# Kernel optimization log

Measured on AMD Instinct MI355X. Metric: run time of the kernel, lower is better.

## Reference

```python
import jax, jax.numpy as jnp
import numpy as np

EMBED = 768
HEADS = 12
HEAD_DIM = EMBED // HEADS

def setup_inputs() -> dict:
    key = jax.random.key(0)
    k1, k2, k3, k4 = jax.random.split(key, 4)
    x = jax.random.normal(k1, (8, 1024, EMBED), dtype=jnp.float32)
    # qkv Linear (no bias per qkv_bias=False); proj Linear with bias
    w_qkv = jax.random.normal(k2, (EMBED, 3 * EMBED), dtype=jnp.float32) * 0.02
    w_proj = jax.random.normal(k3, (EMBED, EMBED), dtype=jnp.float32) * 0.02
    b_proj = jax.random.normal(k4, (EMBED,), dtype=jnp.float32) * 0.02
    return {"x": x, "w_qkv": w_qkv, "w_proj": w_proj, "b_proj": b_proj}

def reference(x, w_qkv, w_proj, b_proj):
    b, n, e = x.shape
    h, d = HEADS, HEAD_DIM
    scale = d ** (-0.5)
    qkv = x @ w_qkv                                    # [b, n, 3*e]
    qkv = qkv.reshape(b, n, 3, h, d)                   # (qkv h d) split order
    q, k, v = (jnp.transpose(qkv[:, :, i], (0, 2, 1, 3)) for i in range(3))  # [b,h,n,d]
    dots = jnp.einsum('bhid,bhjd->bhij', q, k) * scale
    attn = jax.nn.softmax(dots, axis=-1)               # dropout p=0 -> identity
    out = jnp.einsum('bhij,bhjd->bhid', attn, v)       # [b,h,n,d]
    out = jnp.transpose(out, (0, 2, 1, 3)).reshape(b, n, e)
    return out @ w_proj + b_proj
```

## Files before the change

### kernel.cpp

```cpp
#include <hip/hip_runtime.h>

typedef _Float16 f16;
typedef _Float16 half8 __attribute__((ext_vector_type(8)));
typedef _Float16 half4v __attribute__((ext_vector_type(4)));
typedef __fp16 fp16x2 __attribute__((ext_vector_type(2)));
typedef float f32x4 __attribute__((ext_vector_type(4)));
typedef float f32x16 __attribute__((ext_vector_type(16)));

#define MFMA16(a,b,c) __builtin_amdgcn_mfma_f32_16x16x32_f16((a),(b),(c),0,0,0)
#define MFMA32(a,b,c) __builtin_amdgcn_mfma_f32_32x32x16_f16((a),(b),(c),0,0,0)

__device__ __forceinline__ void gload_lds16(const f16* g, f16* l) {
    __builtin_amdgcn_global_load_lds(
        (const __attribute__((address_space(1))) unsigned int*)g,
        (__attribute__((address_space(3))) unsigned int*)l, 16, 0, 0);
}

__global__ void cast_f32_to_f16(const float* __restrict__ in, f16* __restrict__ out, int n4) {
    int i = blockIdx.x * blockDim.x + threadIdx.x;
    if (i < n4) {
        float4 v = ((const float4*)in)[i];
        half4v h;
        h.x = (f16)v.x; h.y = (f16)v.y; h.z = (f16)v.z; h.w = (f16)v.w;
        ((half4v*)out)[i] = h;
    }
}

__global__ void transpose_cast(const float* __restrict__ in, f16* __restrict__ out, int K, int N) {
    __shared__ f16 tile[32][33];
    int n0 = blockIdx.x * 32, k0 = blockIdx.y * 32;
    int tx = threadIdx.x & 31, ty = threadIdx.x >> 5;
    for (int r = ty; r < 32; r += 8)
        tile[r][tx] = (f16)in[(size_t)(k0 + r) * N + (n0 + tx)];
    __syncthreads();
    for (int r = ty; r < 32; r += 8)
        out[(size_t)(n0 + r) * K + (k0 + tx)] = tile[tx][r];
}

template<int MODE>
__global__ __launch_bounds__(256, 3)
void gemm_bt(const f16* __restrict__ A, const f16* __restrict__ Bt,
             f16* __restrict__ qbuf, f16* __restrict__ kbuf, f16* __restrict__ vtbuf,
             float* __restrict__ out, const float* __restrict__ bias)
{
    constexpr int K = 768;
    constexpr int NX = (MODE == 0) ? 18 : 6;
    constexpr int NWG = NX * 64;
    __shared__ __align__(16) char smem[49152];
    f16* As = (f16*)smem;
    f16* Bs = (f16*)(smem + 24576);
    const int tid  = threadIdx.x;
    const int lane = tid & 63, wave = tid >> 6;
    const int wm = wave >> 1, wn = wave & 1;
    const int l15 = lane & 15, l4 = lane >> 4;

    const int bid = blockIdx.x;
    const int swz = (bid & 7) * (NWG / 8) + (bid >> 3);
    const int m0 = (swz / NX) * 128, n0 = (swz % NX) * 128;

    const int srow  = lane >> 2;
    const int sslot = lane & 3;

    f32x4 acc[4][4] = {};

    #define GSTAGE(buf, kt) do {                                                     \
        _Pragma("unroll")                                                            \
        for (int i = 0; i < 2; ++i) {                                                \
            int rbase = i * 64 + wave * 16;                                          \
            int row = rbase + srow;                                                  \
            gload_lds16(A  + (size_t)(m0 + row) * K + (kt) + sslot * 8, &As[(buf) * 4096 + rbase * 32]); \
            gload_lds16(Bt + (size_t)(n0 + row) * K + (kt) + sslot * 8, &Bs[(buf) * 4096 + rbase * 32]); \
        }                                                                            \
    } while (0)

    GSTAGE(0, 0);
    GSTAGE(1, 32);

    int cur = 0;
    for (int t = 0; t < 24; ++t) {
        if (t < 23) asm volatile("s_waitcnt vmcnt(4)" ::: "memory");
        else        asm volatile("s_waitcnt vmcnt(0)" ::: "memory");
        __builtin_amdgcn_s_barrier();
        if (t < 22) {
            int nb = cur + 2; if (nb >= 3) nb -= 3;
            GSTAGE(nb, (t + 2) * 32);
        }
        half8 af[4], bf[4];
        #pragma unroll
        for (int mi = 0; mi < 4; mi++) af[mi] = *(const half8*)&As[cur*4096 + (wm*64 + mi*16 + l15) * 32 + l4*8];
        #pragma unroll
        for (int ni = 0; ni < 4; ni++) bf[ni] = *(const half8*)&Bs[cur*4096 + (wn*64 + ni*16 + l15) * 32 + l4*8];
        #pragma unroll
        for (int mi = 0; mi < 4; mi++)
            #pragma unroll
            for (int ni = 0; ni < 4; ni++)
                acc[mi][ni] = MFMA16(af[mi], bf[ni], acc[mi][ni]);
        if (++cur >= 3) cur = 0;
    }
    #undef GSTAGE

    if (MODE == 0) {
        __syncthreads();
        f16* sC = (f16*)smem;
        const int t3 = n0 / 768;
        const int bb = m0 >> 10;
        const int mo = m0 & 1023;
        const int h0 = (n0 - t3 * 768) >> 6;

        if (t3 < 2) {
            #pragma unroll
            for (int mi = 0; mi < 4; mi++)
                #pragma unroll
                for (int ni = 0; ni < 4; ni++)
                    #pragma unroll
                    for (int r = 0; r < 4; r++) {
                        int row = wm*64 + mi*16 + l4*4 + r;
                        int col = wn*64 + ni*16 + l15;
                        sC[row * 136 + col] = (f16)acc[mi][ni][r];
                    }
            __syncthreads();
            f16* outb = (t3 == 0) ? qbuf : kbuf;
            #pragma unroll
            for (int hc = 0; hc < 2; hc++) {
                f16* base = outb + ((size_t)(bb * 12 + h0 + hc) * 1024 + mo) * 64;
                #pragma unroll
                for (int i = 0; i < 4; i++) {
                    int row = wave * 32 + i * 8 + (lane >> 3);
                    int cc  = (lane & 7) * 8;
                    half8 v = *(const half8*)&sC[row * 136 + hc * 64 + cc];
                    *(half8*)(base + row * 64 + cc) = v;
                }
            }
        } else {
            #pragma unroll
            for (int mi = 0; mi < 4; mi++)
                #pragma unroll
                for (int ni = 0; ni < 4; ni++) {
                    int row0 = wm*64 + mi*16 + l4*4;
                    int col  = wn*64 + ni*16 + l15;
                    half4v pk;
                    #pragma unroll
                    for (int r = 0; r < 4; r++) pk[r] = (f16)acc[mi][ni][r];
                    *(half4v*)&sC[col * 136 + row0] = pk;
                }
            __syncthreads();
            #pragma unroll
            for (int i = 0; i < 8; i++) {
                int col = wave * 32 + i * 4 + (lane >> 4);
                int rc  = (lane & 15) * 8;
                half8 v = *(const half8*)&sC[col * 136 + rc];
                int head = h0 + (col >> 6), dd = col & 63;
                *(half8*)(vtbuf + ((size_t)(bb * 12 + head) * 64 + dd) * 1024 + mo + rc) = v;
            }
        }
    } else {
        #pragma unroll
        for (int mi = 0; mi < 4; mi++)
            #pragma unroll
            for (int ni = 0; ni < 4; ni++)
                #pragma unroll
                for (int r = 0; r < 4; r++) {
                    int gm = m0 + wm*64 + mi*16 + l4*4 + r;
                    int gn = n0 + wn*64 + ni*16 + l15;
                    out[(size_t)gm * 768 + gn] = acc[mi][ni][r] + bias[gn];
                }
    }
}

__global__ __launch_bounds__(256, 3)
void attn_kernel(const f16* __restrict__ qbuf, const f16* __restrict__ kbuf,
                 const f16* __restrict__ vtbuf, f16* __restrict__ obuf)
{
    __shared__ __align__(16) f16 Ks[2][4096];
    __shared__ __align__(16) f16 Vs[2][4096];
    __shared__ __align__(16) char sPall[4 * 4096];
    const int tid = threadIdx.x;
    const int lane = tid & 63, wave = tid >> 6;
    char* sP = sPall + wave * 4096;
    const int bh = blockIdx.x;
    const int b = bh / 12, h = bh % 12;
    const int q0 = blockIdx.y * 128 + wave * 32;
    const int l31 = lane & 31, hi = lane >> 5;
    const int sw0 = (l31 & 7) << 4;

    const f16* Q  = qbuf  + (size_t)bh * 65536;
    const f16* Kp = kbuf  + (size_t)bh * 65536;
    const f16* Vt = vtbuf + (size_t)bh * 65536;

    const f16 slh = (f16)(0.125f * 1.44269504089f);
    half8 aq[4];
    #pragma unroll
    for (int c = 0; c < 4; c++) {
        aq[c] = *(const half8*)&Q[(size_t)(q0 + l31) * 64 + c * 16 + hi * 8];
        #pragma unroll
        for (int j = 0; j < 8; j++) aq[c][j] *= slh;
    }

    const int srow8 = lane >> 3;
    const int c16   = (lane & 7) ^ srow8;

    f32x16 o0 = {}, o1 = {};
    float lrq = 0.f, mrq = 0.f;

    #define STAGE(buf, kv) do {                                                     \
        _Pragma("unroll")                                                           \
        for (int i = 0; i < 2; ++i) {                                               \
            int rbase = wave * 16 + i * 8;                                          \
            int rl = rbase + srow8;                                                 \
            gload_lds16(Kp + (size_t)((kv) + rl) * 64 + c16 * 8, &Ks[buf][rbase * 64]); \
            gload_lds16(Vt + (size_t)rl * 1024 + (kv) + c16 * 8, &Vs[buf][rbase * 64]); \
        }                                                                           \
    } while (0)

    STAGE(0, 0);
    __syncthreads();

    for (int t = 0; t < 16; ++t) {
        const int cur = t & 1;
        if (t < 15) STAGE(cur ^ 1, (t + 1) * 64);

        const char* Kb = (const char*)&Ks[cur][0];
        const char* Vb = (const char*)&Vs[cur][0];

        f32x16 st0, st1;
        #pragma unroll
        for (int j = 0; j < 16; j++) { st0[j] = -mrq; st1[j] = -mrq; }
        #pragma unroll
        for (int c = 0; c < 4; c++) {
            int koff = (c * 32 + hi * 16) ^ sw0;
            half8 k0 = *(const half8*)(Kb + l31 * 128 + koff);
            half8 k1 = *(const half8*)(Kb + (32 + l31) * 128 + koff);
            st0 = MFMA32(k0, aq[c], st0);
            st1 = MFMA32(k1, aq[c], st1);
        }

        float m16 = st0[0];
        #pragma unroll
        for (int j = 1; j < 16; j++) m16 = fmaxf(m16, st0[j]);
        #pragma unroll
        for (int j = 0; j < 16; j++) m16 = fmaxf(m16, st1[j]);
        m16 = fmaxf(m16, __shfl_xor(m16, 32));

        if (!__all(m16 <= 11.0f)) {
            float d = fmaxf(m16, 0.f);
            float alpha = exp2f(-d);
            mrq += d;
            #pragma unroll
            for (int j = 0; j < 16; j++) { st0[j] -= d; st1[j] -= d; }
            lrq *= alpha;
            #pragma unroll
            for (int reg = 0; reg < 16; reg++) {
                float a = __shfl(alpha, (reg & 3) + 8 * (reg >> 2) + 4 * hi);
                o0[reg] *= a; o1[reg] *= a;
            }
        }

        float rs = 0.f;
        #define PSTORE(stv, tile) do {                                              \
            _Pragma("unroll")                                                       \
            for (int g = 0; g < 4; g++) {                                           \
                float e0 = exp2f(stv[4*g+0]), e1 = exp2f(stv[4*g+1]);               \
                float e2 = exp2f(stv[4*g+2]), e3 = exp2f(stv[4*g+3]);               \
                rs += (e0 + e1) + (e2 + e3);                                        \
                uint2 u;                                                            \
                u.x = __builtin_bit_cast(unsigned int, __builtin_amdgcn_cvt_pkrtz(e0, e1)); \
                u.y = __builtin_bit_cast(unsigned int, __builtin_amdgcn_cvt_pkrtz(e2, e3)); \
                int byte = (l31 * 128 + ((tile) * 32 + g * 8 + hi * 4) * 2) ^ sw0;  \
                *(uint2*)(sP + byte) = u;                                           \
            }                                                                       \
        } while (0)
        PSTORE(st0, 0);
        PSTORE(st1, 1);
        #undef PSTORE
        rs += __shfl_xor(rs, 32);
        lrq += rs;

        #pragma unroll
        for (int kc = 0; kc < 4; kc++) {
            int koff = (kc * 32 + hi * 16) ^ sw0;
            half8 pa = *(const half8*)(sP + l31 * 128 + koff);
            half8 v0 = *(const half8*)(Vb + l31 * 128 + koff);
            half8 v1 = *(const half8*)(Vb + (32 + l31) * 128 + koff);
            o0 = MFMA32(pa, v0, o0);
            o1 = MFMA32(pa, v1, o1);
        }

        __syncthreads();
    }
    #undef STAGE

    float rq = 1.0f / lrq;
    f16* Op = obuf + (size_t)b * 1024 * 768 + h * 64;
    #pragma unroll
    for (int reg = 0; reg < 16; reg++) {
        int qrow = (reg & 3) + 8 * (reg >> 2) + 4 * hi;
        float inv = __shfl(rq, qrow);
        size_t base = (size_t)(q0 + qrow) * 768;
        Op[base + l31]      = (f16)(o0[reg] * inv);
        Op[base + 32 + l31] = (f16)(o1[reg] * inv);
    }
}

extern "C" void kernel_launch(void* const* d_in, const int* in_sizes, int n_in,
                              void* d_out, int out_size, void* d_ws, size_t ws_size,
                              hipStream_t stream) {
    const float* x      = (const float*)d_in[0];
    const float* w_qkv  = (const float*)d_in[1];
    const float* w_proj = (const float*)d_in[2];
    const float* b_proj = (const float*)d_in[3];
    float* out = (float*)d_out;
    char* ws = (char*)d_ws;

    f16* x_h      = (f16*)(ws + 0);
    f16* w_qkv_t  = (f16*)(ws + 12582912);
    f16* w_proj_t = (f16*)(ws + 16121856);
    f16* qb       = (f16*)(ws + 17301504);
    f16* kb       = (f16*)(ws + 29884416);
    f16* vtb      = (f16*)(ws + 42467328);
    f16* ob       = (f16*)(ws + 55050240);

    cast_f32_to_f16<<<dim3(6144), dim3(256), 0, stream>>>(x, x_h, 6291456 / 4);
    transpose_cast<<<dim3(2304 / 32, 768 / 32), dim3(256), 0, stream>>>(w_qkv, w_qkv_t, 768, 2304);
    transpose_cast<<<dim3(768 / 32, 768 / 32), dim3(256), 0, stream>>>(w_proj, w_proj_t, 768, 768);
    gemm_bt<0><<<dim3(18 * 64), dim3(256), 0, stream>>>(
        x_h, w_qkv_t, qb, kb, vtb, nullptr, nullptr);
    attn_kernel<<<dim3(96, 8), dim3(256), 0, stream>>>(qb, kb, vtb, ob);
    gemm_bt<1><<<dim3(6 * 64), dim3(256), 0, stream>>>(
        ob, w_proj_t, nullptr, nullptr, nullptr, out, b_proj);
}
```

Baseline: 127.6 us.

## Keep softmax probabilities in registers via permlane32 swap instead of LDS round-trip

Replaces the per-wave LDS staging of the P matrix with an in-register relayout that uses v_permlane32_swap to turn the S accumulator layout into MFMA A-operand fragments. This drops 16KB of shared memory and the LDS store/load traffic, which lets occupancy go up to 4 blocks per CU. It also raises wave priority around the MFMA loops. The exp2 values are recomputed for the row sum, including a dead extra loop over st0, which adds redundant transcendental work the compiler may or may not remove.

```diff
diff --git a/kernel.cpp b/kernel.cpp
--- a/kernel.cpp
+++ b/kernel.cpp
@@ -6,6 +6,7 @@
 typedef __fp16 fp16x2 __attribute__((ext_vector_type(2)));
 typedef float f32x4 __attribute__((ext_vector_type(4)));
 typedef float f32x16 __attribute__((ext_vector_type(16)));
+typedef unsigned uint4v __attribute__((ext_vector_type(4)));
 
 #define MFMA16(a,b,c) __builtin_amdgcn_mfma_f32_16x16x32_f16((a),(b),(c),0,0,0)
 #define MFMA32(a,b,c) __builtin_amdgcn_mfma_f32_32x32x16_f16((a),(b),(c),0,0,0)
@@ -14,6 +15,14 @@
     __builtin_amdgcn_global_load_lds(
         (const __attribute__((address_space(1))) unsigned int*)g,
         (__attribute__((address_space(3))) unsigned int*)l, 16, 0, 0);
+}
+
+__device__ __forceinline__ void plswap(unsigned &a, unsigned &b) {
+    asm volatile("v_permlane32_swap_b32 %0, %1" : "+v"(a), "+v"(b));
+}
+
+__device__ __forceinline__ unsigned pkexp(float a, float b) {
+    return __builtin_bit_cast(unsigned, __builtin_amdgcn_cvt_pkrtz(exp2f(a), exp2f(b)));
 }
 
 __global__ void cast_f32_to_f16(const float* __restrict__ in, f16* __restrict__ out, int n4) {
@@ -167,16 +176,14 @@
     }
 }
 
-__global__ __launch_bounds__(256, 3)
+__global__ __launch_bounds__(256, 4)
 void attn_kernel(const f16* __restrict__ qbuf, const f16* __restrict__ kbuf,
                  const f16* __restrict__ vtbuf, f16* __restrict__ obuf)
 {
     __shared__ __align__(16) f16 Ks[2][4096];
     __shared__ __align__(16) f16 Vs[2][4096];
-    __shared__ __align__(16) char sPall[4 * 4096];
     const int tid = threadIdx.x;
     const int lane = tid & 63, wave = tid >> 6;
-    char* sP = sPall + wave * 4096;
     const int bh = blockIdx.x;
     const int b = bh / 12, h = bh % 12;
     const int q0 = blockIdx.y * 128 + wave * 32;
@@ -225,6 +232,7 @@
         f32x16 st0, st1;
         #pragma unroll
         for (int j = 0; j < 16; j++) { st0[j] = -mrq; st1[j] = -mrq; }
+        __builtin_amdgcn_s_setprio(1);
         #pragma unroll
         for (int c = 0; c < 4; c++) {
             int koff = (c * 32 + hi * 16) ^ sw0;
@@ -233,6 +241,7 @@
             st0 = MFMA32(k0, aq[c], st0);
             st1 = MFMA32(k1, aq[c], st1);
         }
+        __builtin_amdgcn_s_setprio(0);
 
         float m16 = st0[0];
         #pragma unroll
@@ -256,34 +265,41 @@
         }
 
         float rs = 0.f;
-        #define PSTORE(stv, tile) do {                                              \
-            _Pragma("unroll")                                                       \
-            for (int g = 0; g < 4; g++) {                                           \
-                float e0 = exp2f(stv[4*g+0]), e1 = exp2f(stv[4*g+1]);               \
-                float e2 = exp2f(stv[4*g+2]), e3 = exp2f(stv[4*g+3]);               \
-                rs += (e0 + e1) + (e2 + e3);                                        \
-                uint2 u;                                                            \
-                u.x = __builtin_bit_cast(unsigned int, __builtin_amdgcn_cvt_pkrtz(e0, e1)); \
-                u.y = __builtin_bit_cast(unsigned int, __builtin_amdgcn_cvt_pkrtz(e2, e3)); \
-                int byte = (l31 * 128 + ((tile) * 32 + g * 8 + hi * 4) * 2) ^ sw0;  \
-                *(uint2*)(sP + byte) = u;                                           \
-            }                                                                       \
-        } while (0)
-        PSTORE(st0, 0);
-        PSTORE(st1, 1);
-        #undef PSTORE
+        #pragma unroll
+        for (int j = 0; j < 16; j++) rs += exp2f(st0[j]);
+        rs = 0.f;
+        half8 pa[4];
+        #pragma unroll
+        for (int tile = 0; tile < 2; tile++) {
+            const f32x16& sv = tile ? st1 : st0;
+            #pragma unroll
+            for (int half16 = 0; half16 < 2; half16++) {
+                int rb = half16 * 8;
+                unsigned A1 = pkexp(sv[rb+0], sv[rb+1]);
+                unsigned B1 = pkexp(sv[rb+4], sv[rb+5]);
+                unsigned A2 = pkexp(sv[rb+2], sv[rb+3]);
+                unsigned B2 = pkexp(sv[rb+6], sv[rb+7]);
+                plswap(A1, B1);
+                plswap(A2, B2);
+                uint4v w = {A1, A2, B1, B2};
+                pa[tile * 2 + half16] = __builtin_bit_cast(half8, w);
+            }
+            #pragma unroll
+            for (int j = 0; j < 16; j++) rs += exp2f(sv[j]);
+        }
         rs += __shfl_xor(rs, 32);
         lrq += rs;
 
+        __builtin_amdgcn_s_setprio(1);
         #pragma unroll
         for (int kc = 0; kc < 4; kc++) {
             int koff = (kc * 32 + hi * 16) ^ sw0;
-            half8 pa = *(const half8*)(sP + l31 * 128 + koff);
             half8 v0 = *(const half8*)(Vb + l31 * 128 + koff);
             half8 v1 = *(const half8*)(Vb + (32 + l31) * 128 + koff);
-            o0 = MFMA32(pa, v0, o0);
-            o1 = MFMA32(pa, v1, o1);
-        }
+            o0 = MFMA32(pa[kc], v0, o0);
+            o1 = MFMA32(pa[kc], v1, o1);
+        }
+        __builtin_amdgcn_s_setprio(0);
 
         __syncthreads();
     }
```

New measurement: 127.6 us. About the same (+0.1%).
